# Kernel tuning notes

Measured on AMD Instinct MI355X. Metric: run time of the kernel, lower is better.

Reference implementation:

```python
import jax, jax.numpy as jnp
import numpy as np

B, T, C = 16, 1023, 2048
N_LAYER, LAYER_ID = 24, 12


def setup_inputs() -> dict:
    key = jax.random.key(0)
    k0, k1, k2, k3, k4 = jax.random.split(key, 5)
    x = jax.random.normal(k0, (B, T, C), jnp.float32)
    # decay schedule exactly as in RWKV_TimeMix.__init__ (first_sa_layer_id = 1)
    f1 = 3.0 + (LAYER_ID - 1) / (N_LAYER - 2) * (1.2 - 3.0)
    f2 = 0.65 + (LAYER_ID - 1) / (N_LAYER - 2) * (0.4 - 0.65)
    h = np.arange(C, dtype=np.float64)
    decay_speed = np.power(f2, h / (C - 1) * 7) * f1
    time_decay = jnp.asarray(np.log(decay_speed), jnp.float32)          # [C]
    time_first = jnp.full((C,), float(np.log(0.3)), jnp.float32)        # [C]
    time_mix = jnp.concatenate([jnp.zeros((C // 2,), jnp.float32),
                                jnp.ones((C - C // 2,), jnp.float32)])  # [C]
    s = 0.02
    Wk = jax.random.normal(k1, (C, C), jnp.float32) * s
    Wv = jax.random.normal(k2, (C, C), jnp.float32) * s
    Wr = jax.random.normal(k3, (C, C), jnp.float32) * s
    Wo = jax.random.normal(k4, (C, C), jnp.float32) * s
    z = jnp.zeros((B, C), jnp.float32)
    return {"x": x, "time_decay": time_decay, "time_first": time_first,
            "time_mix": time_mix, "Wk": Wk, "Wv": Wv, "Wr": Wr, "Wo": Wo,
            "xx": z, "aa": z, "bb": z, "mm": z}


def reference(x, time_decay, time_first, time_mix, Wk, Wv, Wr, Wo, xx, aa, bb, mm):
    Bn, Tn, Cn = x.shape
    # time_shift: prepend carried last-token state xx, drop last
    x_shift = jnp.concatenate([xx[:, None, :], x[:, :-1, :]], axis=1)
    xm = x * time_mix + x_shift * (1.0 - time_mix)
    k = xm @ Wk.T                       # [B, T, C]
    v = xm @ Wv.T
    r = xm @ Wr.T
    # running-max renorm to the nearest power of two: ldexp(0.5, frexp(max_t k).exponent)
    kmax = jax.lax.stop_gradient(jnp.max(k, axis=1))   # [B, C], max over time
    _, expo = jnp.frexp(kmax)
    mm_new = jnp.ldexp(jnp.float32(0.5), expo)          # [B, C]
    k = jnp.exp(k - mm_new[:, None, :])
    kv = k * v
    # TimeX kernel weights: w[c, T-1-delta] = exp(-exp(time_decay[c]) * (delta-1)) = d**(delta-1),
    # w[c, T-1] = exp(time_first[c]); so wk[t] = e_first*k[t] + sum_{u<t} d^{t-1-u} k[u] -> linear scan
    d = jnp.exp(-jnp.exp(time_decay))                   # [C] per-channel decay (= w[...,-3])
    e_first = jnp.exp(time_first)                       # [C] (w[...,-1])
    rsf = jnp.exp(mm - mm_new)                          # rescale carried state to new renorm
    k_seq = jnp.concatenate([(bb * rsf)[:, None, :], k], axis=1)    # [B, T+1, C]
    kv_seq = jnp.concatenate([(aa * rsf)[:, None, :], kv], axis=1)  # [B, T+1, C]

    def step(carry, inp):
        Sk, Skv = carry
        kt, kvt = inp
        out = (e_first * kt + Sk, e_first * kvt + Skv)
        return (d * Sk + kt, d * Skv + kvt), out

    init = (jnp.zeros((Bn, Cn), x.dtype), jnp.zeros((Bn, Cn), x.dtype))
    seq = (jnp.swapaxes(k_seq, 0, 1), jnp.swapaxes(kv_seq, 0, 1))   # [T+1, B, C]
    _, (wk_s, wkv_s) = jax.lax.scan(step, init, seq)
    wk = jnp.swapaxes(wk_s[1:], 0, 1)     # drop state slot -> [B, T, C]
    wkv = jnp.swapaxes(wkv_s[1:], 0, 1)
    rwkv = jax.nn.sigmoid(r) * jnp.nan_to_num(wkv / wk)
    return rwkv @ Wo.T
```

## Files before the change

### kernel.cpp

```cpp
#include <hip/hip_runtime.h>
#include <hip/hip_bf16.h>
#include <hip/hip_fp16.h>
#include <math.h>
#include <float.h>

#define BB 16
#define TT 1023
#define CC 2048
#define M_ROWS (BB * TT)
#define MP 16384
#define N3 (3 * CC)
#define NCH 16
#define CHL 64

typedef __attribute__((ext_vector_type(8))) short bfrag;
typedef __attribute__((ext_vector_type(4))) float f32x4;
typedef __attribute__((ext_vector_type(4))) short short4v;

__device__ __forceinline__ void async16(const void* g, void* l) {
  __builtin_amdgcn_global_load_lds((const __attribute__((address_space(1))) void*)g,
                                   (__attribute__((address_space(3))) void*)l, 16, 0, 0);
}

__device__ __forceinline__ short bfb(float f) {
  __hip_bfloat16 h = __float2bfloat16(f);
  return *reinterpret_cast<short*>(&h);
}

__global__ void cast_weights(const float* __restrict__ Wk, const float* __restrict__ Wv,
                             const float* __restrict__ Wr, const float* __restrict__ Wo,
                             __hip_bfloat16* __restrict__ W3, __hip_bfloat16* __restrict__ WoB) {
  size_t i4 = (size_t)blockIdx.x * 256 + threadIdx.x;
  size_t i = i4 * 4;
  float4 a = *(const float4*)(Wk + i);
  float4 b = *(const float4*)(Wv + i);
  float4 c = *(const float4*)(Wr + i);
  float4 d = *(const float4*)(Wo + i);
  *(short4v*)((short*)W3 + i)              = short4v{bfb(a.x), bfb(a.y), bfb(a.z), bfb(a.w)};
  *(short4v*)((short*)W3 + i + CC * CC)    = short4v{bfb(b.x), bfb(b.y), bfb(b.z), bfb(b.w)};
  *(short4v*)((short*)W3 + i + 2 * CC * CC) = short4v{bfb(c.x), bfb(c.y), bfb(c.z), bfb(c.w)};
  *(short4v*)((short*)WoB + i)             = short4v{bfb(d.x), bfb(d.y), bfb(d.z), bfb(d.w)};
}

__global__ void build_xm(const float* __restrict__ x, const float* __restrict__ xx,
                         const float* __restrict__ tmix, __hip_bfloat16* __restrict__ xm) {
  int m = blockIdx.x;
  short* orow = (short*)xm + (size_t)m * CC;
  if (m >= M_ROWS) {
    for (int c = threadIdx.x; c < CC / 4; c += 256)
      ((short4v*)orow)[c] = short4v{0, 0, 0, 0};
    return;
  }
  int b = m / TT, t = m - b * TT;
  const float* xrow = x + (size_t)m * CC;
  const float* xprev = (t == 0) ? (xx + (size_t)b * CC) : (xrow - CC);
  for (int c = threadIdx.x; c < CC / 4; c += 256) {
    float4 xv = ((const float4*)xrow)[c];
    float4 pv = ((const float4*)xprev)[c];
    float4 tm = ((const float4*)tmix)[c];
    ((short4v*)orow)[c] = short4v{
        bfb(xv.x * tm.x + pv.x * (1.0f - tm.x)),
        bfb(xv.y * tm.y + pv.y * (1.0f - tm.y)),
        bfb(xv.z * tm.z + pv.z * (1.0f - tm.z)),
        bfb(xv.w * tm.w + pv.w * (1.0f - tm.w))};
  }
}

template <int MODE>
__global__ __launch_bounds__(512, 2)
void gemm256(const short* __restrict__ A, const short* __restrict__ Bw,
             float* __restrict__ outF, __half* __restrict__ outH,
             __hip_bfloat16* __restrict__ outV, __hip_bfloat16* __restrict__ outR) {
  __shared__ short lds[65536];

  const int lane = threadIdx.x & 63, wid = threadIdx.x >> 6;
  const int wr = wid >> 2, wc = wid & 3;

  const int nx = gridDim.x;
  const int nwg = nx * gridDim.y;
  const int bid = blockIdx.y * nx + blockIdx.x;
  const int q = nwg >> 3;
  const int swz = (bid & 7) * q + (bid >> 3);
  const int mBase = (swz / nx) * 256;
  const int nBase = (swz % nx) * 256;

  const int srow = lane >> 2;
  const int scol = (((lane & 3) ^ ((lane >> 3) & 3)) * 8);
  const int stgOff = wid * 1024 + lane * 8;
  const short* aSrcBase = A  + (size_t)(mBase + wid * 32 + srow) * CC + scol;
  const short* bSrcBase = Bw + (size_t)(nBase + wid * 32 + srow) * CC + scol;

  const int ldOff = (lane & 15) * 32 + (((lane >> 4) ^ ((lane >> 1) & 3)) * 8);

  const short* pA0 = lds + wr * 128 * 32 + ldOff;
  const short* pA1 = pA0 + 32768;
  const short* pB0 = lds + 16384 + wc * 64 * 32 + ldOff;
  const short* pB1 = pB0 + 32768;

  f32x4 acc[2][4][4] = {};
  bfrag aqA[4], aqB[4], bqA[4], bqB[4];

#define RGNA(buf, kh) ((buf) * 32768 + (kh) * 8192)
#define RGNB(buf, kh) (16384 + (buf) * 32768 + (kh) * 8192)

#define STG_A(buf, kh, tk) do { \
    const short* _s = aSrcBase + ((tk) * 64 + (kh) * 32); \
    short* _d = lds + RGNA(buf, kh) + stgOff; \
    async16(_s, _d); async16(_s + (size_t)16 * CC, _d + 512); } while (0)

#define STG_B(buf, kh, tk) do { \
    const short* _s = bSrcBase + ((tk) * 64 + (kh) * 32); \
    short* _d = lds + RGNB(buf, kh) + stgOff; \
    async16(_s, _d); async16(_s + (size_t)16 * CC, _d + 512); } while (0)

#define VMN(n) asm volatile("s_waitcnt vmcnt(" #n ")" ::: "memory")

#define PFA(dst, pA, kh, mh) \
    _Pragma("unroll") \
    for (int f = 0; f < 4; ++f) \
      dst[f] = *(const bfrag*)(pA + (kh) * 8192 + ((mh) * 64 + f * 16) * 32);

#define PFB(dst, pB, kh) \
    _Pragma("unroll") \
    for (int n = 0; n < 4; ++n) \
      dst[n] = *(const bfrag*)(pB + (kh) * 8192 + n * 16 * 32);

#define PH(ai, AQ, BQ, PF, STAGE, WAIT) do { \
    PF \
    __builtin_amdgcn_s_setprio(1); \
    _Pragma("unroll") \
    for (int f = 0; f < 4; ++f) \
      _Pragma("unroll") \
      for (int n = 0; n < 4; ++n) \
        acc[ai][f][n] = __builtin_amdgcn_mfma_f32_16x16x32_bf16(AQ[f], BQ[n], acc[ai][f][n], 0, 0, 0); \
    __builtin_amdgcn_s_setprio(0); \
    STAGE; \
    WAIT; \
    __builtin_amdgcn_s_barrier(); } while (0)

  STG_A(0, 0, 0); STG_B(0, 0, 0);
  STG_A(0, 1, 0); STG_B(0, 1, 0);
  STG_A(1, 0, 1); STG_B(1, 0, 1);
  VMN(2);
  __builtin_amdgcn_s_barrier();
  PFA(aqA, pA0, 0, 0)
  PFB(bqA, pB0, 0)

  for (int ti = 0; ti < 30; ti += 2) {
    PH(0, aqA, bqA, PFA(aqB, pA0, 0, 1),                    STG_A(1, 1, ti + 1), VMN(2));
    PH(1, aqB, bqA, PFA(aqA, pA0, 1, 0) PFB(bqB, pB0, 1),   STG_B(1, 1, ti + 1), );
    PH(0, aqA, bqB, PFA(aqB, pA0, 1, 1),                    STG_A(0, 0, ti + 2), VMN(2));
    PH(1, aqB, bqB, PFA(aqA, pA1, 0, 0) PFB(bqA, pB1, 0),   STG_B(0, 0, ti + 2), );
    PH(0, aqA, bqA, PFA(aqB, pA1, 0, 1),                    STG_A(0, 1, ti + 2), VMN(2));
    PH(1, aqB, bqA, PFA(aqA, pA1, 1, 0) PFB(bqB, pB1, 1),   STG_B(0, 1, ti + 2), );
    PH(0, aqA, bqB, PFA(aqB, pA1, 1, 1),                    STG_A(1, 0, ti + 3), VMN(2));
    PH(1, aqB, bqB, PFA(aqA, pA0, 0, 0) PFB(bqA, pB0, 0),   STG_B(1, 0, ti + 3), );
  }
  PH(0, aqA, bqA, PFA(aqB, pA0, 0, 1),                      STG_A(1, 1, 31), VMN(2));
  PH(1, aqB, bqA, PFA(aqA, pA0, 1, 0) PFB(bqB, pB0, 1),     STG_B(1, 1, 31), );
  PH(0, aqA, bqB, PFA(aqB, pA0, 1, 1),                      , VMN(2));
  PH(1, aqB, bqB, PFA(aqA, pA1, 0, 0) PFB(bqA, pB1, 0),     , );
  PH(0, aqA, bqA, PFA(aqB, pA1, 0, 1),                      , VMN(0));
  PH(1, aqB, bqA, PFA(aqA, pA1, 1, 0) PFB(bqB, pB1, 1),     , );
  PH(0, aqA, bqB, PFA(aqB, pA1, 1, 1),                      , );
  {
    __builtin_amdgcn_s_setprio(1);
#pragma unroll
    for (int f = 0; f < 4; ++f)
#pragma unroll
      for (int n = 0; n < 4; ++n)
        acc[1][f][n] = __builtin_amdgcn_mfma_f32_16x16x32_bf16(aqB[f], bqB[n], acc[1][f][n], 0, 0, 0);
    __builtin_amdgcn_s_setprio(0);
  }

#undef PH
#undef PFA
#undef PFB
#undef VMN
#undef STG_A
#undef STG_B
#undef RGNA
#undef RGNB

#pragma unroll
  for (int mh = 0; mh < 2; ++mh)
#pragma unroll
    for (int f = 0; f < 4; ++f) {
      const int row0 = mBase + wr * 128 + mh * 64 + f * 16 + (lane >> 4) * 4;
      const int col0 = nBase + wc * 64 + (lane & 15);
#pragma unroll
      for (int n = 0; n < 4; ++n) {
        const int col = col0 + n * 16;
#pragma unroll
        for (int rr = 0; rr < 4; ++rr) {
          const int row = row0 + rr;
          if (row < M_ROWS) {
            float val = acc[mh][f][n][rr];
            if constexpr (MODE == 0) {
              outF[(size_t)row * CC + col] = val;
            } else {
              if (col < CC)          outH[(size_t)row * CC + col] = __float2half(expf(val));
              else if (col < 2 * CC) outV[(size_t)row * CC + (col - CC)] = __float2bfloat16(val);
              else                   outR[(size_t)row * CC + (col - 2 * CC)] = __float2bfloat16(val);
            }
          }
        }
      }
    }
}

__global__ __launch_bounds__(1024)
void scan_fuse2(const __half* __restrict__ ek, const __hip_bfloat16* __restrict__ v,
                const __hip_bfloat16* __restrict__ r, const float* __restrict__ aa,
                const float* __restrict__ bb, const float* __restrict__ mm,
                const float* __restrict__ tdec, const float* __restrict__ tfir,
                __hip_bfloat16* __restrict__ rwkv) {
  __shared__ float sBk[NCH][64], sBkv[NCH][64], sSk[NCH][64], sSkv[NCH][64];

  const int lane = threadIdx.x & 63, wid = threadIdx.x >> 6;
  const int c = blockIdx.x * 64 + lane;
  const int b = blockIdx.y;
  const int i = b * CC + c;

  const float dexp = expf(tdec[c]);
  const float d    = expf(-dexp);
  const float ef   = expf(tfir[c]);

  const int t0 = wid * CHL;
  const int t1 = (t0 + CHL < TT) ? t0 + CHL : TT;
  const size_t base = (size_t)b * TT * CC + c;

  if (wid < NCH - 1) {
    float Bk = 0.0f, Bkv = 0.0f;
    size_t off = base + (size_t)t0 * CC;
#pragma unroll 4
    for (int t = t0; t < t1; ++t, off += CC) {
      float kk = __half2float(ek[off]);
      float kv = kk * __bfloat162float(v[off]);
      Bk = d * Bk + kk;
      Bkv = d * Bkv + kv;
    }
    sBk[wid][lane] = Bk;
    sBkv[wid][lane] = Bkv;
  }
  __syncthreads();

  if (wid == 0) {
    const float d64 = expf(-dexp * (float)CHL);
    const float sc = expf(mm[i]);
    float S = bb[i] * sc, Sv = aa[i] * sc;
#pragma unroll
    for (int j = 0; j < NCH; ++j) {
      sSk[j][lane] = S;
      sSkv[j][lane] = Sv;
      if (j < NCH - 1) {
        S = d64 * S + sBk[j][lane];
        Sv = d64 * Sv + sBkv[j][lane];
      }
    }
  }
  __syncthreads();

  float S = sSk[wid][lane], Sv = sSkv[wid][lane];
  size_t off = base + (size_t)t0 * CC;
#pragma unroll 4
  for (int t = t0; t < t1; ++t, off += CC) {
    float kk = __half2float(ek[off]);
    float vv = __bfloat162float(v[off]);
    float rv = __bfloat162float(r[off]);
    float kv = kk * vv;
    float wk = ef * kk + S;
    float wkv = ef * kv + Sv;
    S = d * S + kk;
    Sv = d * Sv + kv;
    float ratio = wkv / wk;
    if (isnan(ratio)) ratio = 0.0f;
    else if (isinf(ratio)) ratio = ratio > 0.0f ? FLT_MAX : -FLT_MAX;
    float sig = 1.0f / (1.0f + expf(-rv));
    rwkv[off] = __float2bfloat16(sig * ratio);
  }
}

extern "C" void kernel_launch(void* const* d_in, const int* in_sizes, int n_in,
                              void* d_out, int out_size, void* d_ws, size_t ws_size,
                              hipStream_t stream) {
  const float* x    = (const float*)d_in[0];
  const float* tdec = (const float*)d_in[1];
  const float* tfir = (const float*)d_in[2];
  const float* tmix = (const float*)d_in[3];
  const float* Wk   = (const float*)d_in[4];
  const float* Wv   = (const float*)d_in[5];
  const float* Wr   = (const float*)d_in[6];
  const float* Wo   = (const float*)d_in[7];
  const float* xx   = (const float*)d_in[8];
  const float* aa   = (const float*)d_in[9];
  const float* bb   = (const float*)d_in[10];
  const float* mm   = (const float*)d_in[11];

  char* ws = (char*)d_ws;
  size_t o = 0;
  __hip_bfloat16* W3  = (__hip_bfloat16*)(ws + o); o += (size_t)N3 * CC * 2;
  __hip_bfloat16* WoB = (__hip_bfloat16*)(ws + o); o += (size_t)CC * CC * 2;
  __hip_bfloat16* xmB = (__hip_bfloat16*)(ws + o); o += (size_t)MP * CC * 2;
  __hip_bfloat16* vB  = (__hip_bfloat16*)(ws + o); o += (size_t)MP * CC * 2;
  __hip_bfloat16* rB  = (__hip_bfloat16*)(ws + o); o += (size_t)MP * CC * 2;

  __half* ekH = (__half*)d_out;
  __hip_bfloat16* rwkvB = xmB;

  cast_weights<<<CC * CC / 1024, 256, 0, stream>>>(Wk, Wv, Wr, Wo, W3, WoB);
  build_xm<<<MP, 256, 0, stream>>>(x, xx, tmix, xmB);
  gemm256<1><<<dim3(N3 / 256, MP / 256), 512, 0, stream>>>(
      (const short*)xmB, (const short*)W3, nullptr, ekH, vB, rB);
  scan_fuse2<<<dim3(CC / 64, BB), 1024, 0, stream>>>(ekH, vB, rB, aa, bb, mm,
                                                     tdec, tfir, rwkvB);
  gemm256<0><<<dim3(CC / 256, MP / 256), 512, 0, stream>>>(
      (const short*)rwkvB, (const short*)WoB, (float*)d_out, nullptr, nullptr, nullptr);
}
```

Measured before the change: 709.5 us.

## Switch GEMM inner loop to 32x32x16 MFMA with reworked fragment loads

Replaces the 16x16x32 bf16 MFMA tiling with 32x32x16 MFMA instructions, using f32x16 accumulators and new LDS fragment addressing for the 32-row layout. Fragment loads are no longer software-prefetched a phase ahead. Each phase now loads its operands, issues the stage copy, barriers, then computes, with the vmcnt waits moved to every fourth phase. The aim is fewer MFMA instructions and LDS reads per FLOP. The cost is less overlap between LDS loads and MFMA work and an extra barrier per phase.

Measured after the change: 741.3 us. +4.5%, slower.

```diff
diff --git a/kernel.cpp b/kernel.cpp
--- a/kernel.cpp
+++ b/kernel.cpp
@@ -14,7 +14,7 @@
 #define CHL 64
 
 typedef __attribute__((ext_vector_type(8))) short bfrag;
-typedef __attribute__((ext_vector_type(4))) float f32x4;
+typedef __attribute__((ext_vector_type(16))) float f32x16;
 typedef __attribute__((ext_vector_type(4))) short short4v;
 
 __device__ __forceinline__ void async16(const void* g, void* l) {
@@ -90,15 +90,23 @@
   const short* aSrcBase = A  + (size_t)(mBase + wid * 32 + srow) * CC + scol;
   const short* bSrcBase = Bw + (size_t)(nBase + wid * 32 + srow) * CC + scol;
 
-  const int ldOff = (lane & 15) * 32 + (((lane >> 4) ^ ((lane >> 1) & 3)) * 8);
-
-  const short* pA0 = lds + wr * 128 * 32 + ldOff;
-  const short* pA1 = pA0 + 32768;
-  const short* pB0 = lds + 16384 + wc * 64 * 32 + ldOff;
-  const short* pB1 = pB0 + 32768;
-
-  f32x4 acc[2][4][4] = {};
-  bfrag aqA[4], aqB[4], bqA[4], bqB[4];
+  const int r32 = lane & 31;
+  const int h5  = lane >> 5;
+  const int x3  = (r32 >> 1) & 3;
+  const int ldK0 = r32 * 32 + ((h5 ^ x3) * 8);
+  const int ldK1 = r32 * 32 + (((2 + h5) ^ x3) * 8);
+
+  const short* a0k0 = lds + wr * 128 * 32 + ldK0;
+  const short* a0k1 = lds + wr * 128 * 32 + ldK1;
+  const short* b0k0 = lds + 16384 + wc * 64 * 32 + ldK0;
+  const short* b0k1 = lds + 16384 + wc * 64 * 32 + ldK1;
+  const short* a1k0 = a0k0 + 32768;
+  const short* a1k1 = a0k1 + 32768;
+  const short* b1k0 = b0k0 + 32768;
+  const short* b1k1 = b0k1 + 32768;
+
+  f32x16 acc[4][2] = {};
+  bfrag bq[2][2];
 
 #define RGNA(buf, kh) ((buf) * 32768 + (kh) * 8192)
 #define RGNB(buf, kh) (16384 + (buf) * 32768 + (kh) * 8192)
@@ -115,26 +123,32 @@
 
 #define VMN(n) asm volatile("s_waitcnt vmcnt(" #n ")" ::: "memory")
 
-#define PFA(dst, pA, kh, mh) \
+#define PH(aK0, aK1, bK0, bK1, kh, mh, STAGE, WAIT) do { \
+    bfrag aq[2][2]; \
+    if ((mh) == 0) { \
+      _Pragma("unroll") \
+      for (int nb = 0; nb < 2; ++nb) { \
+        bq[nb][0] = *(const bfrag*)(bK0 + (kh) * 8192 + nb * 1024); \
+        bq[nb][1] = *(const bfrag*)(bK1 + (kh) * 8192 + nb * 1024); \
+      } \
+    } \
     _Pragma("unroll") \
-    for (int f = 0; f < 4; ++f) \
-      dst[f] = *(const bfrag*)(pA + (kh) * 8192 + ((mh) * 64 + f * 16) * 32);
-
-#define PFB(dst, pB, kh) \
-    _Pragma("unroll") \
-    for (int n = 0; n < 4; ++n) \
-      dst[n] = *(const bfrag*)(pB + (kh) * 8192 + n * 16 * 32);
-
-#define PH(ai, AQ, BQ, PF, STAGE, WAIT) do { \
-    PF \
+    for (int mb = 0; mb < 2; ++mb) { \
+      aq[mb][0] = *(const bfrag*)(aK0 + (kh) * 8192 + ((mh) * 64 + mb * 32) * 32); \
+      aq[mb][1] = *(const bfrag*)(aK1 + (kh) * 8192 + ((mh) * 64 + mb * 32) * 32); \
+    } \
+    STAGE; \
+    __builtin_amdgcn_s_barrier(); \
     __builtin_amdgcn_s_setprio(1); \
     _Pragma("unroll") \
-    for (int f = 0; f < 4; ++f) \
+    for (int mb = 0; mb < 2; ++mb) \
       _Pragma("unroll") \
-      for (int n = 0; n < 4; ++n) \
-        acc[ai][f][n] = __builtin_amdgcn_mfma_f32_16x16x32_bf16(AQ[f], BQ[n], acc[ai][f][n], 0, 0, 0); \
+      for (int nb = 0; nb < 2; ++nb) \
+        _Pragma("unroll") \
+        for (int ks = 0; ks < 2; ++ks) \
+          acc[(mh) * 2 + mb][nb] = __builtin_amdgcn_mfma_f32_32x32x16_bf16( \
+              aq[mb][ks], bq[nb][ks], acc[(mh) * 2 + mb][nb], 0, 0, 0); \
     __builtin_amdgcn_s_setprio(0); \
-    STAGE; \
     WAIT; \
     __builtin_amdgcn_s_barrier(); } while (0)
 
@@ -143,39 +157,27 @@
   STG_A(1, 0, 1); STG_B(1, 0, 1);
   VMN(2);
   __builtin_amdgcn_s_barrier();
-  PFA(aqA, pA0, 0, 0)
-  PFB(bqA, pB0, 0)
 
   for (int ti = 0; ti < 30; ti += 2) {
-    PH(0, aqA, bqA, PFA(aqB, pA0, 0, 1),                    STG_A(1, 1, ti + 1), VMN(2));
-    PH(1, aqB, bqA, PFA(aqA, pA0, 1, 0) PFB(bqB, pB0, 1),   STG_B(1, 1, ti + 1), );
-    PH(0, aqA, bqB, PFA(aqB, pA0, 1, 1),                    STG_A(0, 0, ti + 2), VMN(2));
-    PH(1, aqB, bqB, PFA(aqA, pA1, 0, 0) PFB(bqA, pB1, 0),   STG_B(0, 0, ti + 2), );
-    PH(0, aqA, bqA, PFA(aqB, pA1, 0, 1),                    STG_A(0, 1, ti + 2), VMN(2));
-    PH(1, aqB, bqA, PFA(aqA, pA1, 1, 0) PFB(bqB, pB1, 1),   STG_B(0, 1, ti + 2), );
-    PH(0, aqA, bqB, PFA(aqB, pA1, 1, 1),                    STG_A(1, 0, ti + 3), VMN(2));
-    PH(1, aqB, bqB, PFA(aqA, pA0, 0, 0) PFB(bqA, pB0, 0),   STG_B(1, 0, ti + 3), );
-  }
-  PH(0, aqA, bqA, PFA(aqB, pA0, 0, 1),                      STG_A(1, 1, 31), VMN(2));
-  PH(1, aqB, bqA, PFA(aqA, pA0, 1, 0) PFB(bqB, pB0, 1),     STG_B(1, 1, 31), );
-  PH(0, aqA, bqB, PFA(aqB, pA0, 1, 1),                      , VMN(2));
-  PH(1, aqB, bqB, PFA(aqA, pA1, 0, 0) PFB(bqA, pB1, 0),     , );
-  PH(0, aqA, bqA, PFA(aqB, pA1, 0, 1),                      , VMN(0));
-  PH(1, aqB, bqA, PFA(aqA, pA1, 1, 0) PFB(bqB, pB1, 1),     , );
-  PH(0, aqA, bqB, PFA(aqB, pA1, 1, 1),                      , );
-  {
-    __builtin_amdgcn_s_setprio(1);
-#pragma unroll
-    for (int f = 0; f < 4; ++f)
-#pragma unroll
-      for (int n = 0; n < 4; ++n)
-        acc[1][f][n] = __builtin_amdgcn_mfma_f32_16x16x32_bf16(aqB[f], bqB[n], acc[1][f][n], 0, 0, 0);
-    __builtin_amdgcn_s_setprio(0);
-  }
+    PH(a0k0, a0k1, b0k0, b0k1, 0, 0, STG_A(1, 1, ti + 1), );
+    PH(a0k0, a0k1, b0k0, b0k1, 0, 1, STG_B(1, 1, ti + 1), );
+    PH(a0k0, a0k1, b0k0, b0k1, 1, 0, STG_A(0, 0, ti + 2), );
+    PH(a0k0, a0k1, b0k0, b0k1, 1, 1, STG_B(0, 0, ti + 2), VMN(2));
+    PH(a1k0, a1k1, b1k0, b1k1, 0, 0, STG_A(0, 1, ti + 2), );
+    PH(a1k0, a1k1, b1k0, b1k1, 0, 1, STG_B(0, 1, ti + 2), );
+    PH(a1k0, a1k1, b1k0, b1k1, 1, 0, STG_A(1, 0, ti + 3), );
+    PH(a1k0, a1k1, b1k0, b1k1, 1, 1, STG_B(1, 0, ti + 3), VMN(2));
+  }
+  PH(a0k0, a0k1, b0k0, b0k1, 0, 0, STG_A(1, 1, 31), );
+  PH(a0k0, a0k1, b0k0, b0k1, 0, 1, STG_B(1, 1, 31), );
+  PH(a0k0, a0k1, b0k0, b0k1, 1, 0, , );
+  PH(a0k0, a0k1, b0k0, b0k1, 1, 1, , VMN(2));
+  PH(a1k0, a1k1, b1k0, b1k1, 0, 0, , );
+  PH(a1k0, a1k1, b1k0, b1k1, 0, 1, , VMN(0));
+  PH(a1k0, a1k1, b1k0, b1k1, 1, 0, , );
+  PH(a1k0, a1k1, b1k0, b1k1, 1, 1, , );
 
 #undef PH
-#undef PFA
-#undef PFB
 #undef VMN
 #undef STG_A
 #undef STG_B
@@ -183,26 +185,22 @@
 #undef RGNB
 
 #pragma unroll
-  for (int mh = 0; mh < 2; ++mh)
+  for (int mb = 0; mb < 4; ++mb)
 #pragma unroll
-    for (int f = 0; f < 4; ++f) {
-      const int row0 = mBase + wr * 128 + mh * 64 + f * 16 + (lane >> 4) * 4;
-      const int col0 = nBase + wc * 64 + (lane & 15);
+    for (int nb = 0; nb < 2; ++nb) {
+      const int rowb = mBase + wr * 128 + mb * 32 + 4 * h5;
+      const int col  = nBase + wc * 64 + nb * 32 + r32;
 #pragma unroll
-      for (int n = 0; n < 4; ++n) {
-        const int col = col0 + n * 16;
-#pragma unroll
-        for (int rr = 0; rr < 4; ++rr) {
-          const int row = row0 + rr;
-          if (row < M_ROWS) {
-            float val = acc[mh][f][n][rr];
-            if constexpr (MODE == 0) {
-              outF[(size_t)row * CC + col] = val;
-            } else {
-              if (col < CC)          outH[(size_t)row * CC + col] = __float2half(expf(val));
-              else if (col < 2 * CC) outV[(size_t)row * CC + (col - CC)] = __float2bfloat16(val);
-              else                   outR[(size_t)row * CC + (col - 2 * CC)] = __float2bfloat16(val);
-            }
+      for (int reg = 0; reg < 16; ++reg) {
+        const int row = rowb + (reg & 3) + 8 * (reg >> 2);
+        if (row < M_ROWS) {
+          float val = acc[mb][nb][reg];
+          if constexpr (MODE == 0) {
+            outF[(size_t)row * CC + col] = val;
+          } else {
+            if (col < CC)          outH[(size_t)row * CC + col] = __float2half(expf(val));
+            else if (col < 2 * CC) outV[(size_t)row * CC + (col - CC)] = __float2bfloat16(val);
+            else                   outR[(size_t)row * CC + (col - 2 * CC)] = __float2bfloat16(val);
           }
         }
       }
```
